# Kernel optimization log

Measured on AMD Instinct MI355X. Metric: run time of the kernel, lower is better.

Reference implementation:

```python
import jax, jax.numpy as jnp
import numpy as np

B, T, C, HD = 16, 2048, 1024, 64


def setup_inputs() -> dict:
    key = jax.random.key(0)
    kx, kk, kq, kv = jax.random.split(key, 4)
    x = jax.random.normal(kx, (B, T, C), dtype=jnp.float32)
    Wk = jax.random.normal(kk, (C, HD), dtype=jnp.float32) * (C ** -0.5)
    Wq = jax.random.normal(kq, (C, HD), dtype=jnp.float32) * (C ** -0.5)
    Wv = jax.random.normal(kv, (C, HD), dtype=jnp.float32) * (C ** -0.5)
    return {"x": x, "Wk": Wk, "Wq": Wq, "Wv": Wv}


def reference(x, Wk, Wq, Wv):
    Bs, Ts, Cs = x.shape
    k = x @ Wk  # [B,T,HD]
    q = x @ Wq
    v = x @ Wv
    # Faithful to original: scores = key @ query^T, scaled by 1/sqrt(C) (embed dim!)
    scores = jnp.einsum('bth,bsh->bts', k, q) / jnp.sqrt(jnp.float32(Cs))
    causal = jnp.tril(jnp.ones((Ts, Ts), dtype=bool))  # tril[:T,:T]
    scores = jnp.where(causal, scores, -jnp.inf)
    weights = jax.nn.softmax(scores, axis=-1)  # [B,T,T]
    return jnp.einsum('bts,bsh->bth', weights, v)  # [B,T,HD]
```

## Files before the change

### kernel.cpp

```cpp
#include <hip/hip_runtime.h>
#include <hip/hip_bf16.h>

#define B_ 16
#define T_ 2048
#define C_ 1024
#define HD_ 64

typedef __attribute__((ext_vector_type(8))) short bf16x8;
typedef __attribute__((ext_vector_type(4))) float f32x4;

__device__ __forceinline__ unsigned short f2bf(float f) {
  unsigned int u = __builtin_bit_cast(unsigned int, f);
  unsigned int r = (u + 0x7fffu + ((u >> 16) & 1u)) >> 16;
  return (unsigned short)r;
}

__device__ __forceinline__ bf16x8 cvt8(float4 a, float4 b) {
  bf16x8 r;
  r[0] = (short)f2bf(a.x); r[1] = (short)f2bf(a.y);
  r[2] = (short)f2bf(a.z); r[3] = (short)f2bf(a.w);
  r[4] = (short)f2bf(b.x); r[5] = (short)f2bf(b.y);
  r[6] = (short)f2bf(b.z); r[7] = (short)f2bf(b.w);
  return r;
}

__global__ void wconv_kernel(const float* __restrict__ Wk, const float* __restrict__ Wq,
                             const float* __restrict__ Wv, unsigned short* __restrict__ wt) {
  int o = blockIdx.x * 256 + threadIdx.x;
  if (o >= 3 * HD_ * C_) return;
  int m = o >> 16;
  int d = (o >> 10) & 63;
  int c = o & 1023;
  const float* W = (m == 0) ? Wk : (m == 1) ? Wq : Wv;
  wt[o] = f2bf(W[c * HD_ + d]);
}

__global__ __launch_bounds__(256, 5) void qkv_kernel(const float* __restrict__ x,
                                                     const unsigned short* __restrict__ wt,
                                                     unsigned short* __restrict__ kb,
                                                     unsigned short* __restrict__ qb,
                                                     unsigned short* __restrict__ vb) {
  __shared__ __align__(16) unsigned short wl[2 * 6144];

  const int tid = threadIdx.x;
  const int lane = tid & 63;
  const int w = tid >> 6;
  const int l15 = lane & 15;
  const int lh = lane >> 4;
  const int r0 = blockIdx.x * 64;

  const int rb = l15 * 32 + ((lh ^ ((l15 >> 1) & 3)) << 3);

  const float* xp = x + (size_t)(r0 + w * 16 + l15) * C_ + lh * 8;

  f32x4 acc[12];
#pragma unroll
  for (int i = 0; i < 12; ++i) acc[i] = {0.f, 0.f, 0.f, 0.f};

#define STAGE_W(buf, kk)                                                              \
  do {                                                                                \
    _Pragma("unroll")                                                                 \
    for (int i_ = 0; i_ < 3; ++i_) {                                                  \
      const int L_ = (w * 3 + i_) << 10;                  \
      const int d_ = (L_ >> 6) + (lane >> 2);                                         \
      const int kc_ = lane & 3;                                                       \
      const int sw_ = (d_ >> 1) & 3;                                                  \
      const unsigned short* g_ = wt + ((size_t)d_ << 10) + (kk) * 32 + ((kc_ ^ sw_) << 3); \
      __builtin_amdgcn_global_load_lds(                                               \
          (const __attribute__((address_space(1))) void*)g_,                          \
          (__attribute__((address_space(3))) void*)&wl[(buf) * 6144 + (L_ >> 1)],     \
          16, 0, 0);                                                                  \
    }                                                                                 \
  } while (0)

  STAGE_W(0, 0);
  float4 f0 = *reinterpret_cast<const float4*>(xp);
  float4 f1 = *reinterpret_cast<const float4*>(xp + 4);
  __syncthreads();

  for (int kk = 0; kk < 32; ++kk) {
    const int cur = kk & 1;
    if (kk < 31) STAGE_W(cur ^ 1, kk + 1);
    const int koff = (kk < 31) ? (kk + 1) * 32 : kk * 32;
    float4 n0 = *reinterpret_cast<const float4*>(xp + koff);
    float4 n1 = *reinterpret_cast<const float4*>(xp + koff + 4);

    bf16x8 a = cvt8(f0, f1);
    const unsigned short* wbase = &wl[cur * 6144 + rb];
#pragma unroll
    for (int cf = 0; cf < 12; ++cf) {
      bf16x8 bfrag = *reinterpret_cast<const bf16x8*>(wbase + cf * 512);
      acc[cf] = __builtin_amdgcn_mfma_f32_16x16x32_bf16(a, bfrag, acc[cf], 0, 0, 0);
    }
    __syncthreads();
    f0 = n0; f1 = n1;
  }
#undef STAGE_W

#pragma unroll
  for (int cf = 0; cf < 4; ++cf) {
    int col = cf * 16 + l15;
#pragma unroll
    for (int r = 0; r < 4; ++r) {
      size_t row = (size_t)(r0 + w * 16 + lh * 4 + r);
      kb[row * HD_ + col] = f2bf(acc[cf][r] * 0.03125f);
      qb[row * HD_ + col] = f2bf(acc[4 + cf][r]);
      vb[row * HD_ + col] = f2bf(acc[8 + cf][r]);
    }
  }
}

__global__ __launch_bounds__(256) void attn_kernel(const unsigned short* __restrict__ kb,
                                                   const unsigned short* __restrict__ qb,
                                                   const unsigned short* __restrict__ vb,
                                                   float* __restrict__ out) {
  __shared__ __align__(16) unsigned short q_lds[64 * 72];
  __shared__ __align__(16) unsigned short v_lds[64 * 72];
  __shared__ __align__(16) unsigned short p_lds[64 * 72];

  const int tid = threadIdx.x;
  const int lane = tid & 63;
  const int w = tid >> 6;
  const int bid = blockIdx.x;
  const int jt = 31 - (bid >> 4);
  const int b = bid & 15;
  const int t0 = jt * 64;
  const int l15 = lane & 15;
  const int lh = lane >> 4;
  const size_t base = (size_t)b * T_ * HD_;

  bf16x8 kf[2];
#pragma unroll
  for (int ks = 0; ks < 2; ++ks)
    kf[ks] = *reinterpret_cast<const bf16x8*>(
        &kb[base + (size_t)(t0 + w * 16 + l15) * HD_ + ks * 32 + lh * 8]);

  f32x4 o[4];
#pragma unroll
  for (int i = 0; i < 4; ++i) o[i] = {0.f, 0.f, 0.f, 0.f};
  float mrun[4], lrun[4];
#pragma unroll
  for (int r = 0; r < 4; ++r) { mrun[r] = -1e30f; lrun[r] = 0.f; }

  for (int j = 0; j <= jt; ++j) {
    const int s0 = j * 64;
    __syncthreads();
#pragma unroll
    for (int i = 0; i < 2; ++i) {
      int c = i * 256 + tid;
      int row = c >> 3, c8 = c & 7;
      bf16x8 qv = *reinterpret_cast<const bf16x8*>(&qb[base + (size_t)(s0 + row) * HD_ + c8 * 8]);
      *reinterpret_cast<bf16x8*>(&q_lds[row * 72 + c8 * 8]) = qv;
    }
#pragma unroll
    for (int i = 0; i < 2; ++i) {
      int c = i * 256 + tid;
      int ss = c & 63, d0 = (c >> 6) * 8;
      bf16x8 vv = *reinterpret_cast<const bf16x8*>(&vb[base + (size_t)(s0 + ss) * HD_ + d0]);
#pragma unroll
      for (int jj = 0; jj < 8; ++jj) v_lds[(d0 + jj) * 72 + ss] = (unsigned short)vv[jj];
    }
    __syncthreads();

    f32x4 sf[4];
#pragma unroll
    for (int cf = 0; cf < 4; ++cf) sf[cf] = {0.f, 0.f, 0.f, 0.f};
#pragma unroll
    for (int ks = 0; ks < 2; ++ks) {
#pragma unroll
      for (int cf = 0; cf < 4; ++cf) {
        bf16x8 bq = *reinterpret_cast<const bf16x8*>(&q_lds[(cf * 16 + l15) * 72 + ks * 32 + lh * 8]);
        sf[cf] = __builtin_amdgcn_mfma_f32_16x16x32_bf16(kf[ks], bq, sf[cf], 0, 0, 0);
      }
    }

    const bool diag = (j == jt);
    float pv[4][4];
#pragma unroll
    for (int r = 0; r < 4; ++r) {
      const int tg = t0 + w * 16 + lh * 4 + r;
      float pm = -1e30f;
#pragma unroll
      for (int cf = 0; cf < 4; ++cf) {
        float v = sf[cf][r];
        if (diag && (s0 + cf * 16 + l15) > tg) v = -1e30f;
        pv[cf][r] = v;
        pm = fmaxf(pm, v);
      }
      pm = fmaxf(pm, __shfl_xor(pm, 1));
      pm = fmaxf(pm, __shfl_xor(pm, 2));
      pm = fmaxf(pm, __shfl_xor(pm, 4));
      pm = fmaxf(pm, __shfl_xor(pm, 8));
      float mn = fmaxf(mrun[r], pm);
      float scl = __expf(mrun[r] - mn);
      mrun[r] = mn;
      float rs = 0.f;
#pragma unroll
      for (int cf = 0; cf < 4; ++cf) {
        float e = __expf(pv[cf][r] - mn);
        pv[cf][r] = e;
        rs += e;
      }
      rs += __shfl_xor(rs, 1);
      rs += __shfl_xor(rs, 2);
      rs += __shfl_xor(rs, 4);
      rs += __shfl_xor(rs, 8);
      lrun[r] = lrun[r] * scl + rs;
#pragma unroll
      for (int df = 0; df < 4; ++df) o[df][r] *= scl;
    }
#pragma unroll
    for (int cf = 0; cf < 4; ++cf)
#pragma unroll
      for (int r = 0; r < 4; ++r)
        p_lds[(w * 16 + lh * 4 + r) * 72 + cf * 16 + l15] = f2bf(pv[cf][r]);
    __syncthreads();

#pragma unroll
    for (int ks = 0; ks < 2; ++ks) {
      bf16x8 pa = *reinterpret_cast<const bf16x8*>(&p_lds[(w * 16 + l15) * 72 + ks * 32 + lh * 8]);
#pragma unroll
      for (int df = 0; df < 4; ++df) {
        bf16x8 bv = *reinterpret_cast<const bf16x8*>(&v_lds[(df * 16 + l15) * 72 + ks * 32 + lh * 8]);
        o[df] = __builtin_amdgcn_mfma_f32_16x16x32_bf16(pa, bv, o[df], 0, 0, 0);
      }
    }
  }

#pragma unroll
  for (int r = 0; r < 4; ++r) {
    float inv = 1.f / lrun[r];
    int row = t0 + w * 16 + lh * 4 + r;
#pragma unroll
    for (int df = 0; df < 4; ++df)
      out[base + (size_t)row * HD_ + df * 16 + l15] = o[df][r] * inv;
  }
}

extern "C" void kernel_launch(void* const* d_in, const int* in_sizes, int n_in,
                              void* d_out, int out_size, void* d_ws, size_t ws_size,
                              hipStream_t stream) {
  const float* x  = (const float*)d_in[0];
  const float* Wk = (const float*)d_in[1];
  const float* Wq = (const float*)d_in[2];
  const float* Wv = (const float*)d_in[3];
  float* out = (float*)d_out;

  char* ws = (char*)d_ws;
  unsigned short* wt = (unsigned short*)ws;
  unsigned short* kb = (unsigned short*)(ws + 524288);
  unsigned short* qb = (unsigned short*)(ws + 524288 + 4 * 1024 * 1024);
  unsigned short* vb = (unsigned short*)(ws + 524288 + 8 * 1024 * 1024);

  hipLaunchKernelGGL(wconv_kernel, dim3(768), dim3(256), 0, stream, Wk, Wq, Wv, wt);
  hipLaunchKernelGGL(qkv_kernel, dim3(512), dim3(256), 0, stream, x, wt, kb, qb, vb);
  hipLaunchKernelGGL(attn_kernel, dim3(512), dim3(256), 0, stream, kb, qb, vb, out);
}
```

Measured before the change: 99.56 us.

## Restructure QKV projection with 64-wide K tiles, pre-swizzled weights, deeper x prefetch

The weight conversion kernel now writes weights pre-swizzled in a layout that matches the LDS bank pattern and folds the key scale into Wk. The QKV GEMM switches to 64-element K tiles (16 iterations instead of 32) with double-buffered LDS and x loads prefetched two iterations ahead. The loop is fully unrolled with explicit vmcnt waits, raw s_barrier calls and sched_barrier hints. It aims to cut barrier and loop overhead and to hide global load latency, but doubles LDS use and lowers the occupancy hint from 5 to 2.

```diff
diff --git a/kernel.cpp b/kernel.cpp
--- a/kernel.cpp
+++ b/kernel.cpp
@@ -10,9 +10,7 @@
 typedef __attribute__((ext_vector_type(4))) float f32x4;
 
 __device__ __forceinline__ unsigned short f2bf(float f) {
-  unsigned int u = __builtin_bit_cast(unsigned int, f);
-  unsigned int r = (u + 0x7fffu + ((u >> 16) & 1u)) >> 16;
-  return (unsigned short)r;
+  return __builtin_bit_cast(unsigned short, __float2bfloat16(f));
 }
 
 __device__ __forceinline__ bf16x8 cvt8(float4 a, float4 b) {
@@ -25,22 +23,26 @@
 }
 
 __global__ void wconv_kernel(const float* __restrict__ Wk, const float* __restrict__ Wq,
-                             const float* __restrict__ Wv, unsigned short* __restrict__ wt) {
+                             const float* __restrict__ Wv, unsigned short* __restrict__ wt2) {
   int o = blockIdx.x * 256 + threadIdx.x;
   if (o >= 3 * HD_ * C_) return;
-  int m = o >> 16;
-  int d = (o >> 10) & 63;
+  int r = o >> 10;
   int c = o & 1023;
+  int s = c >> 3, e = c & 7;
+  int lc = (((s & 0x78) | ((s ^ r) & 7)) << 3) | e;
+  int m = r >> 6, d = r & 63;
   const float* W = (m == 0) ? Wk : (m == 1) ? Wq : Wv;
-  wt[o] = f2bf(W[c * HD_ + d]);
-}
-
-__global__ __launch_bounds__(256, 5) void qkv_kernel(const float* __restrict__ x,
-                                                     const unsigned short* __restrict__ wt,
+  float v = W[lc * HD_ + d];
+  if (m == 0) v *= 0.03125f;
+  wt2[o] = f2bf(v);
+}
+
+__global__ __launch_bounds__(256, 2) void qkv_kernel(const float* __restrict__ x,
+                                                     const unsigned short* __restrict__ wt2,
                                                      unsigned short* __restrict__ kb,
                                                      unsigned short* __restrict__ qb,
                                                      unsigned short* __restrict__ vb) {
-  __shared__ __align__(16) unsigned short wl[2 * 6144];
+  __shared__ __align__(16) unsigned short wl[2 * 12288];
 
   const int tid = threadIdx.x;
   const int lane = tid & 63;
@@ -48,8 +50,9 @@
   const int l15 = lane & 15;
   const int lh = lane >> 4;
   const int r0 = blockIdx.x * 64;
-
-  const int rb = l15 * 32 + ((lh ^ ((l15 >> 1) & 3)) << 3);
+  const int sw = l15 & 7;
+  const int c0 = (lh ^ sw) * 8;
+  const int c1 = ((4 | lh) ^ sw) * 8;
 
   const float* xp = x + (size_t)(r0 + w * 16 + l15) * C_ + lh * 8;
 
@@ -57,45 +60,91 @@
 #pragma unroll
   for (int i = 0; i < 12; ++i) acc[i] = {0.f, 0.f, 0.f, 0.f};
 
-#define STAGE_W(buf, kk)                                                              \
-  do {                                                                                \
-    _Pragma("unroll")                                                                 \
-    for (int i_ = 0; i_ < 3; ++i_) {                                                  \
-      const int L_ = (w * 3 + i_) << 10;                  \
-      const int d_ = (L_ >> 6) + (lane >> 2);                                         \
-      const int kc_ = lane & 3;                                                       \
-      const int sw_ = (d_ >> 1) & 3;                                                  \
-      const unsigned short* g_ = wt + ((size_t)d_ << 10) + (kk) * 32 + ((kc_ ^ sw_) << 3); \
-      __builtin_amdgcn_global_load_lds(                                               \
-          (const __attribute__((address_space(1))) void*)g_,                          \
-          (__attribute__((address_space(3))) void*)&wl[(buf) * 6144 + (L_ >> 1)],     \
-          16, 0, 0);                                                                  \
-    }                                                                                 \
+  float4 xr0[4], xr1[4], xr2[4];
+
+#define STAGE(BUF, KK)                                                               \
+  do {                                                                               \
+    _Pragma("unroll")                                                                \
+    for (int i_ = 0; i_ < 6; ++i_) {                                                 \
+      const int gp_ = w * 6 + i_;                                                    \
+      const int row_ = gp_ * 8 + (lane >> 3);                                        \
+      const unsigned short* g_ = wt2 + row_ * 1024 + (KK) * 64 + (lane & 7) * 8;     \
+      __builtin_amdgcn_global_load_lds(                                              \
+          (const __attribute__((address_space(1))) void*)g_,                         \
+          (__attribute__((address_space(3))) void*)&wl[(BUF) * 12288 + gp_ * 512],   \
+          16, 0, 0);                                                                 \
+    }                                                                                \
   } while (0)
 
-  STAGE_W(0, 0);
-  float4 f0 = *reinterpret_cast<const float4*>(xp);
-  float4 f1 = *reinterpret_cast<const float4*>(xp + 4);
-  __syncthreads();
-
-  for (int kk = 0; kk < 32; ++kk) {
-    const int cur = kk & 1;
-    if (kk < 31) STAGE_W(cur ^ 1, kk + 1);
-    const int koff = (kk < 31) ? (kk + 1) * 32 : kk * 32;
-    float4 n0 = *reinterpret_cast<const float4*>(xp + koff);
-    float4 n1 = *reinterpret_cast<const float4*>(xp + koff + 4);
-
-    bf16x8 a = cvt8(f0, f1);
-    const unsigned short* wbase = &wl[cur * 6144 + rb];
-#pragma unroll
-    for (int cf = 0; cf < 12; ++cf) {
-      bf16x8 bfrag = *reinterpret_cast<const bf16x8*>(wbase + cf * 512);
-      acc[cf] = __builtin_amdgcn_mfma_f32_16x16x32_bf16(a, bfrag, acc[cf], 0, 0, 0);
-    }
-    __syncthreads();
-    f0 = n0; f1 = n1;
-  }
-#undef STAGE_W
+#define XLOAD(XR, KK)                               \
+  do {                                              \
+    const float* p_ = xp + (KK) * 64;               \
+    XR[0] = *(const float4*)(p_);                   \
+    XR[1] = *(const float4*)(p_ + 4);               \
+    XR[2] = *(const float4*)(p_ + 32);              \
+    XR[3] = *(const float4*)(p_ + 36);              \
+  } while (0)
+
+#define COMPUTE(K, XR)                                                                   \
+  do {                                                                                   \
+    const unsigned short* wb = &wl[((K) & 1) * 12288];                                   \
+    bf16x8 a0 = cvt8(XR[0], XR[1]);                                                      \
+    bf16x8 a1 = cvt8(XR[2], XR[3]);                                                      \
+    _Pragma("unroll")                                                                    \
+    for (int cf = 0; cf < 12; ++cf) {                                                    \
+      bf16x8 b0 = *(const bf16x8*)&wb[((cf >> 2) * 64 + (cf & 3) * 16 + l15) * 64 + c0]; \
+      acc[cf] = __builtin_amdgcn_mfma_f32_16x16x32_bf16(a0, b0, acc[cf], 0, 0, 0);       \
+    }                                                                                    \
+    _Pragma("unroll")                                                                    \
+    for (int cf = 0; cf < 12; ++cf) {                                                    \
+      bf16x8 b1 = *(const bf16x8*)&wb[((cf >> 2) * 64 + (cf & 3) * 16 + l15) * 64 + c1]; \
+      acc[cf] = __builtin_amdgcn_mfma_f32_16x16x32_bf16(a1, b1, acc[cf], 0, 0, 0);       \
+    }                                                                                    \
+  } while (0)
+
+#define SB __builtin_amdgcn_sched_barrier(0)
+
+#define ITER(K, XCUR, XPRE, VM)                                    \
+  do {                                                             \
+    if ((K) < 15) STAGE(((K) + 1) & 1, (K) + 1);                   \
+    SB;                                                            \
+    if ((K) < 14) XLOAD(XPRE, (K) + 2);                            \
+    SB;                                                            \
+    asm volatile("s_waitcnt vmcnt(" #VM ")" ::: "memory");         \
+    SB;                                                            \
+    __builtin_amdgcn_s_barrier();                                  \
+    COMPUTE(K, XCUR);                                              \
+    __builtin_amdgcn_s_barrier();                                  \
+  } while (0)
+
+  STAGE(0, 0);
+  SB;
+  XLOAD(xr0, 0);
+  XLOAD(xr1, 1);
+  SB;
+
+  ITER(0, xr0, xr2, 14);
+  ITER(1, xr1, xr0, 14);
+  ITER(2, xr2, xr1, 14);
+  ITER(3, xr0, xr2, 14);
+  ITER(4, xr1, xr0, 14);
+  ITER(5, xr2, xr1, 14);
+  ITER(6, xr0, xr2, 14);
+  ITER(7, xr1, xr0, 14);
+  ITER(8, xr2, xr1, 14);
+  ITER(9, xr0, xr2, 14);
+  ITER(10, xr1, xr0, 14);
+  ITER(11, xr2, xr1, 14);
+  ITER(12, xr0, xr2, 14);
+  ITER(13, xr1, xr0, 14);
+  ITER(14, xr2, xr1, 10);
+  ITER(15, xr0, xr2, 0);
+
+#undef ITER
+#undef COMPUTE
+#undef XLOAD
+#undef STAGE
+#undef SB
 
 #pragma unroll
   for (int cf = 0; cf < 4; ++cf) {
@@ -103,7 +152,7 @@
 #pragma unroll
     for (int r = 0; r < 4; ++r) {
       size_t row = (size_t)(r0 + w * 16 + lh * 4 + r);
-      kb[row * HD_ + col] = f2bf(acc[cf][r] * 0.03125f);
+      kb[row * HD_ + col] = f2bf(acc[cf][r]);
       qb[row * HD_ + col] = f2bf(acc[4 + cf][r]);
       vb[row * HD_ + col] = f2bf(acc[8 + cf][r]);
     }
@@ -247,12 +296,12 @@
   float* out = (float*)d_out;
 
   char* ws = (char*)d_ws;
-  unsigned short* wt = (unsigned short*)ws;
+  unsigned short* wt2 = (unsigned short*)ws;
   unsigned short* kb = (unsigned short*)(ws + 524288);
   unsigned short* qb = (unsigned short*)(ws + 524288 + 4 * 1024 * 1024);
   unsigned short* vb = (unsigned short*)(ws + 524288 + 8 * 1024 * 1024);
 
-  hipLaunchKernelGGL(wconv_kernel, dim3(768), dim3(256), 0, stream, Wk, Wq, Wv, wt);
-  hipLaunchKernelGGL(qkv_kernel, dim3(512), dim3(256), 0, stream, x, wt, kb, qb, vb);
+  hipLaunchKernelGGL(wconv_kernel, dim3(768), dim3(256), 0, stream, Wk, Wq, Wv, wt2);
+  hipLaunchKernelGGL(qkv_kernel, dim3(512), dim3(256), 0, stream, x, wt2, kb, qb, vb);
   hipLaunchKernelGGL(attn_kernel, dim3(512), dim3(256), 0, stream, kb, qb, vb, out);
 }
```

Measured after the change: 94.18 us. -5.4%, faster.
